# Optimization experiments

Hardware: AMD Instinct MI355X
Metric: run time of the kernel (lower is better)

Reference implementation:

```python
import jax, jax.numpy as jnp
import numpy as np

H_DIM = 256
NUM_HEADS = 8
HEAD_DIM = H_DIM // NUM_HEADS
BN_EPS = 1e-5
SCALE = float(np.sqrt(HEAD_DIM))


def _lens():
    # 512 graphs, ragged vertex counts cycling 32/64/96/128 -> 40960 total rows
    return np.tile(np.array([32, 64, 96, 128], dtype=np.int64), 128)


def _pad(x, lens):
    # gather ragged rows of x [total, D] into padded [B, Lmax, D]; mask [B, Lmax]
    B = lens.shape[0]
    L = int(lens.max())
    off = np.zeros(B, np.int64)
    off[1:] = np.cumsum(lens)[:-1]
    pos = np.arange(L)
    idx = off[:, None] + np.minimum(pos[None, :], lens[:, None] - 1)
    mask = pos[None, :] < lens[:, None]
    return x[jnp.asarray(idx)], jnp.asarray(mask)


def _flat_idx(lens):
    # (graph_id, position) for every real row, to un-pad back to ragged layout
    b = np.repeat(np.arange(lens.shape[0]), lens)
    i = np.concatenate([np.arange(int(l)) for l in lens])
    return jnp.asarray(b), jnp.asarray(i)


def _forward(src_h, dst_h, src_lens, dst_lens,
             W1, b1, gamma1, beta1, W2, b2, gamma2, beta2):
    src_pad, src_mask = _pad(src_h, src_lens)   # [B, Ls, H]
    dst_pad, _ = _pad(dst_h, dst_lens)          # [B, Ld, H]
    B, Ls, _ = src_pad.shape
    Ld = dst_pad.shape[1]
    # NOTE: original torch code zips self.proj but never applies it, so
    # q = raw dst, k = v = raw src.  The .view(1, head_dim, heads, N) on the
    # channel-major tensor splits feature f as f = d*NUM_HEADS + h.
    q = dst_pad.reshape(B, Ld, HEAD_DIM, NUM_HEADS)
    k = src_pad.reshape(B, Ls, HEAD_DIM, NUM_HEADS)
    v = k
    scores = jnp.einsum('bndh,bmdh->bhnm', q, k) / SCALE
    scores = jnp.where(src_mask[:, None, None, :], scores, jnp.float32(-1e30))
    attn = jax.nn.softmax(scores, axis=-1)
    out = jnp.einsum('bhnm,bmdh->bndh', attn, v).reshape(B, Ld, H_DIM)
    bidx, iidx = _flat_idx(dst_lens)
    h_msg = out[bidx, iidx]                     # [total_dst, H] ragged again
    h = dst_h
    z = jnp.concatenate([h, h_msg], axis=-1)    # [N, 2H]
    y = z @ W1.T + b1
    y = gamma1 * (y - y.mean(0)) * jax.lax.rsqrt(y.var(0) + BN_EPS) + beta1
    y = jax.nn.relu(y)
    y = y @ W2.T + b2
    y = gamma2 * (y - y.mean(0)) * jax.lax.rsqrt(y.var(0) + BN_EPS) + beta2
    return h + y


def setup_inputs() -> dict:
    lens = _lens()
    N = int(lens.sum())
    ks = jax.random.split(jax.random.key(0), 4)
    return {
        'src_h': jax.random.normal(ks[0], (N, H_DIM), jnp.float32),
        'dst_h': jax.random.normal(ks[1], (N, H_DIM), jnp.float32),
        'src_num_verts': jnp.asarray(lens, jnp.int32),
        'dst_num_verts': jnp.asarray(lens, jnp.int32),
        'W1': jax.random.normal(ks[2], (H_DIM, 2 * H_DIM), jnp.float32) / np.float32(np.sqrt(2 * H_DIM)),
        'b1': jnp.zeros((H_DIM,), jnp.float32),
        'gamma1': jnp.ones((H_DIM,), jnp.float32),
        'beta1': jnp.zeros((H_DIM,), jnp.float32),
        'W2': jax.random.normal(ks[3], (H_DIM, H_DIM), jnp.float32) / np.float32(np.sqrt(H_DIM)),
        'b2': jnp.zeros((H_DIM,), jnp.float32),
        'gamma2': jnp.ones((H_DIM,), jnp.float32),
        'beta2': jnp.zeros((H_DIM,), jnp.float32),
    }


def reference(src_h, dst_h, src_num_verts, dst_num_verts,
              W1, b1, gamma1, beta1, W2, b2, gamma2, beta2):
    # segment lengths are static metadata (torch.split takes a Python list)
    src_lens = np.asarray(jax.device_get(src_num_verts), np.int64)
    dst_lens = np.asarray(jax.device_get(dst_num_verts), np.int64)
    return _forward(src_h, dst_h, src_lens, dst_lens,
                    W1, b1, gamma1, beta1, W2, b2, gamma2, beta2)
```

## Files before the change

### kernel.cpp

```cpp
#include <hip/hip_runtime.h>
#include <cstddef>

#define H 256
#define NHEADS 8
#define HD 32

typedef __attribute__((ext_vector_type(8))) short bf16x8;
typedef __attribute__((ext_vector_type(4))) float f32x4;

__device__ __forceinline__ float bf2f(unsigned short s) {
    unsigned u = ((unsigned)s) << 16; return __builtin_bit_cast(float, u);
}
__device__ __forceinline__ float bfe2f(short s) {
    unsigned u = ((unsigned)(unsigned short)s) << 16; return __builtin_bit_cast(float, u);
}
__device__ __forceinline__ unsigned short f2bf(float x) {
    unsigned u = __builtin_bit_cast(unsigned, x);
    u += 0x7fffu + ((u >> 16) & 1u);
    return (unsigned short)(u >> 16);
}
__device__ __forceinline__ void gl_lds16(const void* g, void* l) {
    __builtin_amdgcn_global_load_lds(
        (const __attribute__((address_space(1))) void*)g,
        (__attribute__((address_space(3))) void*)l, 16, 0, 0);
}

__global__ __launch_bounds__(512) void scan_zero_kernel(
    const int* __restrict__ slen, const int* __restrict__ dlen,
    int* __restrict__ soff, int* __restrict__ doff,
    float* __restrict__ stats, int B)
{
    __shared__ int ss[512], dd[512];
    const int t = threadIdx.x;
    const int sv = (t < B) ? slen[t] : 0;
    const int dv = (t < B) ? dlen[t] : 0;
    ss[t] = sv; dd[t] = dv;
    __syncthreads();
    for (int o = 1; o < 512; o <<= 1) {
        int a = (t >= o) ? ss[t - o] : 0;
        int b = (t >= o) ? dd[t - o] : 0;
        __syncthreads();
        ss[t] += a; dd[t] += b;
        __syncthreads();
    }
    if (t < B) { soff[t] = ss[t] - sv; doff[t] = dd[t] - dv; }
    stats[t] = 0.f;
    stats[t + 512] = 0.f;
}

#define PS 2568
__global__ __launch_bounds__(256) void prepass_kernel(
    const float* __restrict__ src, const float* __restrict__ dst,
    unsigned short* __restrict__ KT, unsigned short* __restrict__ VT2,
    unsigned short* __restrict__ QT, int N)
{
    __shared__ unsigned short pl[8 * PS];
    const int t = threadIdx.x;
    const int rb = blockIdx.x * 64;
    const int isrc = (blockIdx.y == 0);
    const float* __restrict__ in = isrc ? src : dst;
    unsigned short* __restrict__ T = isrc ? KT : QT;
    #pragma unroll
    for (int i = 0; i < 16; ++i) {
        const int idx = t + i * 256;
        const int row = idx >> 6, f4 = idx & 63;
        const float4 v = ((const float4*)in)[(size_t)(rb + row) * 64 + f4];
        const int f0 = f4 * 4, h0 = f0 & 7, d = f0 >> 3;
        pl[(h0 + 0) * PS + row * 40 + d] = f2bf(v.x);
        pl[(h0 + 1) * PS + row * 40 + d] = f2bf(v.y);
        pl[(h0 + 2) * PS + row * 40 + d] = f2bf(v.z);
        pl[(h0 + 3) * PS + row * 40 + d] = f2bf(v.w);
    }
    __syncthreads();
    #pragma unroll
    for (int i = 0; i < 8; ++i) {
        const int idx = t + i * 256;
        const int h = idx >> 8, rem = idx & 255, row = rem >> 2, c = rem & 3;
        const bf16x8 val = *(const bf16x8*)&pl[h * PS + row * 40 + c * 8];
        *(bf16x8*)&T[(size_t)(h * N + rb + row) * 32 + c * 8] = val;
    }
    if (isrc) {
        #pragma unroll
        for (int i = 0; i < 8; ++i) {
            const int idx = t + i * 256;
            const int h = idx >> 8, rem = idx & 255, d = rem >> 3, nc = rem & 7;
            bf16x8 v8;
            #pragma unroll
            for (int j = 0; j < 8; ++j)
                v8[j] = (short)pl[h * PS + (nc * 8 + j) * 40 + d];
            *(bf16x8*)&VT2[(size_t)(h * 32 + d) * N + rb + nc * 8] = v8;
        }
    }
}

__global__ __launch_bounds__(256) void cvtW_kernel(
    const float* __restrict__ W1, const float* __restrict__ W2,
    unsigned short* __restrict__ W1p, unsigned short* __restrict__ W2bf)
{
    const int idx = blockIdx.x * 256 + threadIdx.x;
    if (idx < 131072) {
        const int kp = idx & 511, c = idx >> 9;
        const int half = kp >> 8, r = kp & 255, hh = r >> 5, d = r & 31;
        W1p[(size_t)c * 512 + kp] = f2bf(W1[(size_t)c * 512 + half * 256 + d * 8 + hh]);
    } else {
        const int i2 = idx - 131072;
        W2bf[i2] = f2bf(W2[i2]);
    }
}

template<int LS>
__device__ __forceinline__ void attn_body(
    const unsigned short* __restrict__ KT, const unsigned short* __restrict__ QT,
    const unsigned short* __restrict__ VT2, unsigned short* __restrict__ OT,
    unsigned short* __restrict__ Ps, int N, int so, int df, int Ld, int h, int lane)
{
    constexpr int MT = LS / 16, CH = LS / 32;
    const int lr = lane & 15, lq = lane >> 4;
    const float iscale = 0.17677669529663687f;

    bf16x8 kf[MT];
    #pragma unroll
    for (int mt = 0; mt < MT; ++mt)
        kf[mt] = *(const bf16x8*)&KT[(size_t)(h * N + so + mt * 16 + lr) * 32 + lq * 8];
    bf16x8 vf[CH][2];
    #pragma unroll
    for (int c = 0; c < CH; ++c)
        #pragma unroll
        for (int dt = 0; dt < 2; ++dt)
            vf[c][dt] = *(const bf16x8*)&VT2[(size_t)(h * 32 + dt * 16 + lr) * N + so + c * 32 + lq * 8];

    const int NT = Ld >> 4;
    bf16x8 qf = *(const bf16x8*)&QT[(size_t)(h * N + df + lr) * 32 + lq * 8];
    for (int nt = 0; nt < NT; ++nt) {
        bf16x8 qn = qf;
        if (nt + 1 < NT)
            qn = *(const bf16x8*)&QT[(size_t)(h * N + df + (nt + 1) * 16 + lr) * 32 + lq * 8];
        f32x4 s[MT];
        #pragma unroll
        for (int mt = 0; mt < MT; ++mt) {
            f32x4 z = {0.f, 0.f, 0.f, 0.f};
            s[mt] = __builtin_amdgcn_mfma_f32_16x16x32_bf16(kf[mt], qf, z, 0, 0, 0);
        }
        float mx = -INFINITY;
        #pragma unroll
        for (int mt = 0; mt < MT; ++mt)
            mx = fmaxf(mx, fmaxf(fmaxf(s[mt][0], s[mt][1]), fmaxf(s[mt][2], s[mt][3])));
        mx = fmaxf(mx, __shfl_xor(mx, 16));
        mx = fmaxf(mx, __shfl_xor(mx, 32));
        const float mxi = mx * iscale;
        float sum = 0.f;
        #pragma unroll
        for (int mt = 0; mt < MT; ++mt) {
            #pragma unroll
            for (int r = 0; r < 4; ++r) {
                const float e = __expf(s[mt][r] * iscale - mxi);
                s[mt][r] = e; sum += e;
            }
        }
        sum += __shfl_xor(sum, 16);
        sum += __shfl_xor(sum, 32);
        const float rinv = 1.f / sum;
        #pragma unroll
        for (int mt = 0; mt < MT; ++mt) {
            uint2 p;
            p.x = ((unsigned)f2bf(s[mt][0])) | (((unsigned)f2bf(s[mt][1])) << 16);
            p.y = ((unsigned)f2bf(s[mt][2])) | (((unsigned)f2bf(s[mt][3])) << 16);
            *(uint2*)&Ps[lr * 136 + mt * 16 + lq * 4] = p;
        }
        __asm__ volatile("" ::: "memory");
        __builtin_amdgcn_wave_barrier();
        f32x4 o0 = {0.f, 0.f, 0.f, 0.f}, o1 = {0.f, 0.f, 0.f, 0.f};
        #pragma unroll
        for (int c = 0; c < CH; ++c) {
            const bf16x8 pa = *(const bf16x8*)&Ps[lr * 136 + c * 32 + lq * 8];
            o0 = __builtin_amdgcn_mfma_f32_16x16x32_bf16(pa, vf[c][0], o0, 0, 0, 0);
            o1 = __builtin_amdgcn_mfma_f32_16x16x32_bf16(pa, vf[c][1], o1, 0, 0, 0);
        }
        __asm__ volatile("" ::: "memory");
        __builtin_amdgcn_wave_barrier();
        #pragma unroll
        for (int r = 0; r < 4; ++r) {
            const float rv = __shfl(rinv, lq * 4 + r);
            const int row = df + nt * 16 + lq * 4 + r;
            OT[(size_t)(h * N + row) * 32 + lr]      = f2bf(o0[r] * rv);
            OT[(size_t)(h * N + row) * 32 + 16 + lr] = f2bf(o1[r] * rv);
        }
        qf = qn;
    }
}

__global__ __launch_bounds__(256) void attn_mfma(
    const unsigned short* __restrict__ KT, const unsigned short* __restrict__ QT,
    const unsigned short* __restrict__ VT2, unsigned short* __restrict__ OT,
    const int* __restrict__ soff, const int* __restrict__ doff,
    const int* __restrict__ slen, const int* __restrict__ dlen, int N)
{
    __shared__ unsigned short Ps[4][16 * 136];
    const int i = blockIdx.x >> 1, half = blockIdx.x & 1;
    const int grp = i >> 7, j = i & 127;
    const int b = 4 * j + (3 - grp);
    const int w = threadIdx.x >> 6, lane = threadIdx.x & 63;
    const int h = half * 4 + w;
    const int Ls = slen[b], Ld = dlen[b], so = soff[b], df = doff[b];
    switch (Ls) {
        case 32:  attn_body<32> (KT, QT, VT2, OT, Ps[w], N, so, df, Ld, h, lane); break;
        case 64:  attn_body<64> (KT, QT, VT2, OT, Ps[w], N, so, df, Ld, h, lane); break;
        case 96:  attn_body<96> (KT, QT, VT2, OT, Ps[w], N, so, df, Ld, h, lane); break;
        default:  attn_body<128>(KT, QT, VT2, OT, Ps[w], N, so, df, Ld, h, lane); break;
    }
}

__global__ __launch_bounds__(256) void gemm1_mfma(
    const unsigned short* __restrict__ QT, const unsigned short* __restrict__ OT,
    const unsigned short* __restrict__ W, const float* __restrict__ bias,
    unsigned short* __restrict__ out, float* __restrict__ sum, float* __restrict__ sq,
    int N)
{
    __shared__ unsigned short Abuf[2][4 * 512];
    __shared__ unsigned short Bbuf[2][8 * 512];
    const int tid = threadIdx.x;
    const int w = tid >> 6, lane = tid & 63;
    const int rowBase = blockIdx.y * 64, colBase = blockIdx.x * 128;
    const int lr = lane & 15, lq = lane >> 4;

    f32x4 acc[4][2];
    #pragma unroll
    for (int i = 0; i < 4; ++i)
        #pragma unroll
        for (int j = 0; j < 2; ++j) { f32x4 z = {0.f, 0.f, 0.f, 0.f}; acc[i][j] = z; }

    auto stage = [&](int ks, int bi) {
        const unsigned short* __restrict__ Ap = (ks < 8) ? QT : OT;
        const int hh = ks & 7;
        gl_lds16(Ap + (size_t)(hh * N + rowBase + w * 16 + lr) * 32 + lq * 8,
                 &Abuf[bi][w * 512]);
        #pragma unroll
        for (int s = 0; s < 2; ++s) {
            const int sub = 2 * w + s;
            gl_lds16(W + (size_t)(colBase + sub * 16 + lr) * 512 + ks * 32 + lq * 8,
                     &Bbuf[bi][sub * 512]);
        }
    };
    auto compute = [&](int bi) {
        bf16x8 af[4], bfr[2];
        #pragma unroll
        for (int i = 0; i < 4; ++i) af[i] = *(const bf16x8*)&Abuf[bi][i * 512 + lane * 8];
        #pragma unroll
        for (int j = 0; j < 2; ++j) bfr[j] = *(const bf16x8*)&Bbuf[bi][(w * 2 + j) * 512 + lane * 8];
        #pragma unroll
        for (int i = 0; i < 4; ++i)
            #pragma unroll
            for (int j = 0; j < 2; ++j)
                acc[i][j] = __builtin_amdgcn_mfma_f32_16x16x32_bf16(af[i], bfr[j], acc[i][j], 0, 0, 0);
    };

    stage(0, 0);
    __syncthreads();
    for (int ks = 0; ks < 16; ks += 2) {
        stage(ks + 1, 1);
        compute(0);
        __syncthreads();
        if (ks + 2 < 16) stage(ks + 2, 0);
        compute(1);
        __syncthreads();
    }

    const int col0 = colBase + w * 32;
    #pragma unroll
    for (int j = 0; j < 2; ++j) {
        const int col = col0 + j * 16 + lr;
        const float bv = bias[col];
        float cs = 0.f, cq = 0.f;
        #pragma unroll
        for (int i = 0; i < 4; ++i) {
            const int row0 = rowBase + i * 16 + lq * 4;
            #pragma unroll
            for (int r = 0; r < 4; ++r) {
                const float v = acc[i][j][r] + bv;
                cs += v; cq += v * v;
                out[(size_t)(row0 + r) * 256 + col] = f2bf(v);
            }
        }
        cs += __shfl_xor(cs, 16); cs += __shfl_xor(cs, 32);
        cq += __shfl_xor(cq, 16); cq += __shfl_xor(cq, 32);
        if (lq == 0) { atomicAdd(&sum[col], cs); atomicAdd(&sq[col], cq); }
    }
}

__global__ __launch_bounds__(256) void gemm2_mfma(
    const unsigned short* __restrict__ A2,
    const unsigned short* __restrict__ W, const float* __restrict__ bias,
    unsigned short* __restrict__ out, float* __restrict__ sum, float* __restrict__ sq)
{
    __shared__ unsigned short Abuf[2][4 * 512];
    __shared__ unsigned short Bbuf[2][8 * 512];
    const int tid = threadIdx.x;
    const int w = tid >> 6, lane = tid & 63;
    const int rowBase = blockIdx.y * 64, colBase = blockIdx.x * 128;
    const int lr = lane & 15, lq = lane >> 4;

    f32x4 acc[4][2];
    #pragma unroll
    for (int i = 0; i < 4; ++i)
        #pragma unroll
        for (int j = 0; j < 2; ++j) { f32x4 z = {0.f, 0.f, 0.f, 0.f}; acc[i][j] = z; }

    auto stage = [&](int ks, int bi) {
        gl_lds16(A2 + (size_t)(rowBase + w * 16 + lr) * 256 + ks * 32 + lq * 8,
                 &Abuf[bi][w * 512]);
        #pragma unroll
        for (int s = 0; s < 2; ++s) {
            const int sub = 2 * w + s;
            gl_lds16(W + (size_t)(colBase + sub * 16 + lr) * 256 + ks * 32 + lq * 8,
                     &Bbuf[bi][sub * 512]);
        }
    };
    auto compute = [&](int bi) {
        bf16x8 af[4], bfr[2];
        #pragma unroll
        for (int i = 0; i < 4; ++i) af[i] = *(const bf16x8*)&Abuf[bi][i * 512 + lane * 8];
        #pragma unroll
        for (int j = 0; j < 2; ++j) bfr[j] = *(const bf16x8*)&Bbuf[bi][(w * 2 + j) * 512 + lane * 8];
        #pragma unroll
        for (int i = 0; i < 4; ++i)
            #pragma unroll
            for (int j = 0; j < 2; ++j)
                acc[i][j] = __builtin_amdgcn_mfma_f32_16x16x32_bf16(af[i], bfr[j], acc[i][j], 0, 0, 0);
    };

    stage(0, 0);
    __syncthreads();
    for (int ks = 0; ks < 8; ks += 2) {
        stage(ks + 1, 1);
        compute(0);
        __syncthreads();
        if (ks + 2 < 8) stage(ks + 2, 0);
        compute(1);
        __syncthreads();
    }

    const int col0 = colBase + w * 32;
    #pragma unroll
    for (int j = 0; j < 2; ++j) {
        const int col = col0 + j * 16 + lr;
        const float bv = bias[col];
        float cs = 0.f, cq = 0.f;
        #pragma unroll
        for (int i = 0; i < 4; ++i) {
            const int row0 = rowBase + i * 16 + lq * 4;
            #pragma unroll
            for (int r = 0; r < 4; ++r) {
                const float v = acc[i][j][r] + bv;
                cs += v; cq += v * v;
                out[(size_t)(row0 + r) * 256 + col] = f2bf(v);
            }
        }
        cs += __shfl_xor(cs, 16); cs += __shfl_xor(cs, 32);
        cq += __shfl_xor(cq, 16); cq += __shfl_xor(cq, 32);
        if (lq == 0) { atomicAdd(&sum[col], cs); atomicAdd(&sq[col], cq); }
    }
}

__global__ __launch_bounds__(256) void bnrelu_kernel(
    const unsigned short* __restrict__ y1,
    const float* __restrict__ sum, const float* __restrict__ sq,
    const float* __restrict__ gamma, const float* __restrict__ beta,
    unsigned short* __restrict__ out, int n8, float invN)
{
    const int i = blockIdx.x * 256 + threadIdx.x;
    if (i >= n8) return;
    const int j0 = (i & 31) * 8;
    const bf16x8 yv = ((const bf16x8*)y1)[i];
    short res[8];
    #pragma unroll
    for (int j = 0; j < 8; ++j) {
        const float mean = sum[j0 + j] * invN;
        const float var  = sq[j0 + j] * invN - mean * mean;
        const float rstd = rsqrtf(var + 1e-5f);
        const float sc = gamma[j0 + j] * rstd;
        const float sh = beta[j0 + j] - mean * sc;
        res[j] = (short)f2bf(fmaxf(bfe2f(yv[j]) * sc + sh, 0.f));
    }
    bf16x8 o;
    #pragma unroll
    for (int j = 0; j < 8; ++j) o[j] = res[j];
    ((bf16x8*)out)[i] = o;
}

__global__ __launch_bounds__(256) void epilogue_kernel(
    const float* __restrict__ dst, const unsigned short* __restrict__ y2,
    const float* __restrict__ sum, const float* __restrict__ sq,
    const float* __restrict__ gamma, const float* __restrict__ beta,
    float* __restrict__ out, int n8, float invN)
{
    const int i = blockIdx.x * 256 + threadIdx.x;
    if (i >= n8) return;
    const int j0 = (i & 31) * 8;
    const bf16x8 yv = ((const bf16x8*)y2)[i];
    const float4 d0 = ((const float4*)dst)[2 * i];
    const float4 d1 = ((const float4*)dst)[2 * i + 1];
    float o[8];
    const float dv[8] = {d0.x, d0.y, d0.z, d0.w, d1.x, d1.y, d1.z, d1.w};
    #pragma unroll
    for (int j = 0; j < 8; ++j) {
        const float mean = sum[j0 + j] * invN;
        const float var  = sq[j0 + j] * invN - mean * mean;
        const float rstd = rsqrtf(var + 1e-5f);
        const float sc = gamma[j0 + j] * rstd;
        const float sh = beta[j0 + j] - mean * sc;
        o[j] = dv[j] + bfe2f(yv[j]) * sc + sh;
    }
    float4 o0, o1;
    o0.x = o[0]; o0.y = o[1]; o0.z = o[2]; o0.w = o[3];
    o1.x = o[4]; o1.y = o[5]; o1.z = o[6]; o1.w = o[7];
    ((float4*)out)[2 * i]     = o0;
    ((float4*)out)[2 * i + 1] = o1;
}

extern "C" void kernel_launch(void* const* d_in, const int* in_sizes, int n_in,
                              void* d_out, int out_size, void* d_ws, size_t ws_size,
                              hipStream_t stream)
{
    const float* src_h  = (const float*)d_in[0];
    const float* dst_h  = (const float*)d_in[1];
    const int*   slen   = (const int*)d_in[2];
    const int*   dlen   = (const int*)d_in[3];
    const float* W1     = (const float*)d_in[4];
    const float* b1     = (const float*)d_in[5];
    const float* gamma1 = (const float*)d_in[6];
    const float* beta1  = (const float*)d_in[7];
    const float* W2     = (const float*)d_in[8];
    const float* b2     = (const float*)d_in[9];
    const float* gamma2 = (const float*)d_in[10];
    const float* beta2  = (const float*)d_in[11];
    float* out = (float*)d_out;

    const int N = in_sizes[1] / H;
    const int B = in_sizes[2];

    char* base = (char*)d_ws;
    int*   soff   = (int*)(base + 0);
    int*   doff   = (int*)(base + 2048);
    float* stats  = (float*)(base + 4096);
    unsigned short* W1p  = (unsigned short*)(base + 16384);
    unsigned short* W2bf = (unsigned short*)(base + 16384 + 262144);
    const size_t S = (size_t)N * H * sizeof(unsigned short);
    char* big = base + (1 << 20);
    unsigned short* KT  = (unsigned short*)(big);
    unsigned short* VT2 = (unsigned short*)(big + S);
    unsigned short* QT  = (unsigned short*)(big + 2 * S);
    unsigned short* OT  = (unsigned short*)(big + 3 * S);
    unsigned short* y1bf = KT;
    unsigned short* a2   = VT2;
    unsigned short* y2bf = QT;

    const float invN = 1.0f / (float)N;

    scan_zero_kernel<<<1, 512, 0, stream>>>(slen, dlen, soff, doff, stats, B);

    prepass_kernel<<<dim3(N / 64, 2), 256, 0, stream>>>(src_h, dst_h, KT, VT2, QT, N);
    cvtW_kernel<<<768, 256, 0, stream>>>(W1, W2, W1p, W2bf);

    attn_mfma<<<B * 2, 256, 0, stream>>>(KT, QT, VT2, OT, soff, doff, slen, dlen, N);

    dim3 ggrid(H / 128, N / 64);
    gemm1_mfma<<<ggrid, 256, 0, stream>>>(QT, OT, W1p, b1, y1bf, stats + 0, stats + 256, N);

    const int n8 = N * H / 8;
    bnrelu_kernel<<<(n8 + 255) / 256, 256, 0, stream>>>(
        y1bf, stats + 0, stats + 256, gamma1, beta1, a2, n8, invN);

    gemm2_mfma<<<ggrid, 256, 0, stream>>>(a2, W2bf, b2, y2bf, stats + 512, stats + 768);

    epilogue_kernel<<<(n8 + 255) / 256, 256, 0, stream>>>(
        dst_h, y2bf, stats + 512, stats + 768, gamma2, beta2, out, n8, invN);
}
```

Measured before the change: 276.0 us.

## Restructure GEMMs to register-tiled 160-row blocks without LDS staging

Both MLP GEMM kernels drop the double-buffered LDS staging through global_load_lds. Each wave now loads its weight fragments straight into registers and streams A fragments from global memory, accumulating a 160x32 tile per wave (10x2 MFMA tiles). The grid becomes 512 blocks, each covering 160 rows by 128 columns, so there are fewer blocks and fewer atomics, and weights are reused across more rows. In exchange, all four waves read the same A rows from global memory with no LDS sharing, and the 80 accumulator registers per lane raise register pressure and lower occupancy.

```diff
diff --git a/kernel.cpp b/kernel.cpp
--- a/kernel.cpp
+++ b/kernel.cpp
@@ -18,11 +18,6 @@
     unsigned u = __builtin_bit_cast(unsigned, x);
     u += 0x7fffu + ((u >> 16) & 1u);
     return (unsigned short)(u >> 16);
-}
-__device__ __forceinline__ void gl_lds16(const void* g, void* l) {
-    __builtin_amdgcn_global_load_lds(
-        (const __attribute__((address_space(1))) void*)g,
-        (__attribute__((address_space(3))) void*)l, 16, 0, 0);
 }
 
 __global__ __launch_bounds__(512) void scan_zero_kernel(
@@ -216,69 +211,52 @@
     unsigned short* __restrict__ out, float* __restrict__ sum, float* __restrict__ sq,
     int N)
 {
-    __shared__ unsigned short Abuf[2][4 * 512];
-    __shared__ unsigned short Bbuf[2][8 * 512];
-    const int tid = threadIdx.x;
-    const int w = tid >> 6, lane = tid & 63;
-    const int rowBase = blockIdx.y * 64, colBase = blockIdx.x * 128;
+    const int w = threadIdx.x >> 6, lane = threadIdx.x & 63;
     const int lr = lane & 15, lq = lane >> 4;
-
-    f32x4 acc[4][2];
-    #pragma unroll
-    for (int i = 0; i < 4; ++i)
-        #pragma unroll
-        for (int j = 0; j < 2; ++j) { f32x4 z = {0.f, 0.f, 0.f, 0.f}; acc[i][j] = z; }
-
-    auto stage = [&](int ks, int bi) {
-        const unsigned short* __restrict__ Ap = (ks < 8) ? QT : OT;
-        const int hh = ks & 7;
-        gl_lds16(Ap + (size_t)(hh * N + rowBase + w * 16 + lr) * 32 + lq * 8,
-                 &Abuf[bi][w * 512]);
-        #pragma unroll
-        for (int s = 0; s < 2; ++s) {
-            const int sub = 2 * w + s;
-            gl_lds16(W + (size_t)(colBase + sub * 16 + lr) * 512 + ks * 32 + lq * 8,
-                     &Bbuf[bi][sub * 512]);
-        }
-    };
-    auto compute = [&](int bi) {
-        bf16x8 af[4], bfr[2];
-        #pragma unroll
-        for (int i = 0; i < 4; ++i) af[i] = *(const bf16x8*)&Abuf[bi][i * 512 + lane * 8];
-        #pragma unroll
-        for (int j = 0; j < 2; ++j) bfr[j] = *(const bf16x8*)&Bbuf[bi][(w * 2 + j) * 512 + lane * 8];
-        #pragma unroll
-        for (int i = 0; i < 4; ++i)
-            #pragma unroll
-            for (int j = 0; j < 2; ++j)
-                acc[i][j] = __builtin_amdgcn_mfma_f32_16x16x32_bf16(af[i], bfr[j], acc[i][j], 0, 0, 0);
-    };
-
-    stage(0, 0);
-    __syncthreads();
-    for (int ks = 0; ks < 16; ks += 2) {
-        stage(ks + 1, 1);
-        compute(0);
-        __syncthreads();
-        if (ks + 2 < 16) stage(ks + 2, 0);
-        compute(1);
-        __syncthreads();
-    }
-
-    const int col0 = colBase + w * 32;
-    #pragma unroll
-    for (int j = 0; j < 2; ++j) {
-        const int col = col0 + j * 16 + lr;
+    const int rg = blockIdx.x >> 1, cb = blockIdx.x & 1;
+    const int rs = rg * 160;
+    const int colbase = cb * 128 + w * 32;
+
+    f32x4 acc[10][2];
+    #pragma unroll
+    for (int mt = 0; mt < 10; ++mt)
+        #pragma unroll
+        for (int cf = 0; cf < 2; ++cf) { f32x4 z = {0.f, 0.f, 0.f, 0.f}; acc[mt][cf] = z; }
+
+    #pragma unroll
+    for (int p = 0; p < 8; ++p) {
+        bf16x8 bfr[2][2];
+        #pragma unroll
+        for (int ks = 0; ks < 2; ++ks)
+            #pragma unroll
+            for (int cf = 0; cf < 2; ++cf)
+                bfr[ks][cf] = *(const bf16x8*)&W[(size_t)(colbase + cf * 16 + lr) * 512
+                                                 + (p * 2 + ks) * 32 + lq * 8];
+        const unsigned short* __restrict__ Ap = (p < 4) ? QT : OT;
+        #pragma unroll
+        for (int mt = 0; mt < 10; ++mt) {
+            #pragma unroll
+            for (int ks = 0; ks < 2; ++ks) {
+                const int hh = (p * 2 + ks) & 7;
+                const bf16x8 af = *(const bf16x8*)&Ap[(size_t)(hh * N + rs + mt * 16 + lr) * 32 + lq * 8];
+                acc[mt][0] = __builtin_amdgcn_mfma_f32_16x16x32_bf16(af, bfr[ks][0], acc[mt][0], 0, 0, 0);
+                acc[mt][1] = __builtin_amdgcn_mfma_f32_16x16x32_bf16(af, bfr[ks][1], acc[mt][1], 0, 0, 0);
+            }
+        }
+    }
+
+    #pragma unroll
+    for (int cf = 0; cf < 2; ++cf) {
+        const int col = colbase + cf * 16 + lr;
         const float bv = bias[col];
         float cs = 0.f, cq = 0.f;
         #pragma unroll
-        for (int i = 0; i < 4; ++i) {
-            const int row0 = rowBase + i * 16 + lq * 4;
+        for (int mt = 0; mt < 10; ++mt) {
             #pragma unroll
             for (int r = 0; r < 4; ++r) {
-                const float v = acc[i][j][r] + bv;
+                const float v = acc[mt][cf][r] + bv;
                 cs += v; cq += v * v;
-                out[(size_t)(row0 + r) * 256 + col] = f2bf(v);
+                out[(size_t)(rs + mt * 16 + lq * 4 + r) * 256 + col] = f2bf(v);
             }
         }
         cs += __shfl_xor(cs, 16); cs += __shfl_xor(cs, 32);
@@ -292,67 +270,51 @@
     const unsigned short* __restrict__ W, const float* __restrict__ bias,
     unsigned short* __restrict__ out, float* __restrict__ sum, float* __restrict__ sq)
 {
-    __shared__ unsigned short Abuf[2][4 * 512];
-    __shared__ unsigned short Bbuf[2][8 * 512];
-    const int tid = threadIdx.x;
-    const int w = tid >> 6, lane = tid & 63;
-    const int rowBase = blockIdx.y * 64, colBase = blockIdx.x * 128;
+    const int w = threadIdx.x >> 6, lane = threadIdx.x & 63;
     const int lr = lane & 15, lq = lane >> 4;
-
-    f32x4 acc[4][2];
-    #pragma unroll
-    for (int i = 0; i < 4; ++i)
-        #pragma unroll
-        for (int j = 0; j < 2; ++j) { f32x4 z = {0.f, 0.f, 0.f, 0.f}; acc[i][j] = z; }
-
-    auto stage = [&](int ks, int bi) {
-        gl_lds16(A2 + (size_t)(rowBase + w * 16 + lr) * 256 + ks * 32 + lq * 8,
-                 &Abuf[bi][w * 512]);
-        #pragma unroll
-        for (int s = 0; s < 2; ++s) {
-            const int sub = 2 * w + s;
-            gl_lds16(W + (size_t)(colBase + sub * 16 + lr) * 256 + ks * 32 + lq * 8,
-                     &Bbuf[bi][sub * 512]);
-        }
-    };
-    auto compute = [&](int bi) {
-        bf16x8 af[4], bfr[2];
-        #pragma unroll
-        for (int i = 0; i < 4; ++i) af[i] = *(const bf16x8*)&Abuf[bi][i * 512 + lane * 8];
-        #pragma unroll
-        for (int j = 0; j < 2; ++j) bfr[j] = *(const bf16x8*)&Bbuf[bi][(w * 2 + j) * 512 + lane * 8];
-        #pragma unroll
-        for (int i = 0; i < 4; ++i)
-            #pragma unroll
-            for (int j = 0; j < 2; ++j)
-                acc[i][j] = __builtin_amdgcn_mfma_f32_16x16x32_bf16(af[i], bfr[j], acc[i][j], 0, 0, 0);
-    };
-
-    stage(0, 0);
-    __syncthreads();
-    for (int ks = 0; ks < 8; ks += 2) {
-        stage(ks + 1, 1);
-        compute(0);
-        __syncthreads();
-        if (ks + 2 < 8) stage(ks + 2, 0);
-        compute(1);
-        __syncthreads();
-    }
-
-    const int col0 = colBase + w * 32;
-    #pragma unroll
-    for (int j = 0; j < 2; ++j) {
-        const int col = col0 + j * 16 + lr;
+    const int rg = blockIdx.x >> 1, cb = blockIdx.x & 1;
+    const int rs = rg * 160;
+    const int colbase = cb * 128 + w * 32;
+
+    f32x4 acc[10][2];
+    #pragma unroll
+    for (int mt = 0; mt < 10; ++mt)
+        #pragma unroll
+        for (int cf = 0; cf < 2; ++cf) { f32x4 z = {0.f, 0.f, 0.f, 0.f}; acc[mt][cf] = z; }
+
+    #pragma unroll
+    for (int p = 0; p < 4; ++p) {
+        bf16x8 bfr[2][2];
+        #pragma unroll
+        for (int ks = 0; ks < 2; ++ks)
+            #pragma unroll
+            for (int cf = 0; cf < 2; ++cf)
+                bfr[ks][cf] = *(const bf16x8*)&W[(size_t)(colbase + cf * 16 + lr) * 256
+                                                 + (p * 2 + ks) * 32 + lq * 8];
+        #pragma unroll
+        for (int mt = 0; mt < 10; ++mt) {
+            #pragma unroll
+            for (int ks = 0; ks < 2; ++ks) {
+                const bf16x8 af = *(const bf16x8*)&A2[(size_t)(rs + mt * 16 + lr) * 256
+                                                      + (p * 2 + ks) * 32 + lq * 8];
+                acc[mt][0] = __builtin_amdgcn_mfma_f32_16x16x32_bf16(af, bfr[ks][0], acc[mt][0], 0, 0, 0);
+                acc[mt][1] = __builtin_amdgcn_mfma_f32_16x16x32_bf16(af, bfr[ks][1], acc[mt][1], 0, 0, 0);
+            }
+        }
+    }
+
+    #pragma unroll
+    for (int cf = 0; cf < 2; ++cf) {
+        const int col = colbase + cf * 16 + lr;
         const float bv = bias[col];
         float cs = 0.f, cq = 0.f;
         #pragma unroll
-        for (int i = 0; i < 4; ++i) {
-            const int row0 = rowBase + i * 16 + lq * 4;
+        for (int mt = 0; mt < 10; ++mt) {
             #pragma unroll
             for (int r = 0; r < 4; ++r) {
-                const float v = acc[i][j][r] + bv;
+                const float v = acc[mt][cf][r] + bv;
                 cs += v; cq += v * v;
-                out[(size_t)(row0 + r) * 256 + col] = f2bf(v);
+                out[(size_t)(rs + mt * 16 + lq * 4 + r) * 256 + col] = f2bf(v);
             }
         }
         cs += __shfl_xor(cs, 16); cs += __shfl_xor(cs, 32);
@@ -463,14 +425,13 @@
 
     attn_mfma<<<B * 2, 256, 0, stream>>>(KT, QT, VT2, OT, soff, doff, slen, dlen, N);
 
-    dim3 ggrid(H / 128, N / 64);
-    gemm1_mfma<<<ggrid, 256, 0, stream>>>(QT, OT, W1p, b1, y1bf, stats + 0, stats + 256, N);
+    gemm1_mfma<<<512, 256, 0, stream>>>(QT, OT, W1p, b1, y1bf, stats + 0, stats + 256, N);
 
     const int n8 = N * H / 8;
     bnrelu_kernel<<<(n8 + 255) / 256, 256, 0, stream>>>(
         y1bf, stats + 0, stats + 256, gamma1, beta1, a2, n8, invN);
 
-    gemm2_mfma<<<ggrid, 256, 0, stream>>>(a2, W2bf, b2, y2bf, stats + 512, stats + 768);
+    gemm2_mfma<<<512, 256, 0, stream>>>(a2, W2bf, b2, y2bf, stats + 512, stats + 768);
 
     epilogue_kernel<<<(n8 + 255) / 256, 256, 0, stream>>>(
         dst_h, y2bf, stats + 512, stats + 768, gamma2, beta2, out, n8, invN);
```

New measurement: 269.6 us. 1.02x faster.
